# Optimization experiments

Measured on AMD Instinct MI355X. Metric: run time of the kernel, lower is better.

Reference implementation:

```python
import jax, jax.numpy as jnp
import numpy as np

D_MODEL = 512
NHEAD = 8


def setup_inputs() -> dict:
    key = jax.random.key(0)
    ks = jax.random.split(key, 8)
    d = D_MODEL
    low_feats = jax.random.normal(ks[0], (1, d, 32, 32), dtype=jnp.float32)
    guide_feats = jax.random.normal(ks[1], (1, d, 128, 128), dtype=jnp.float32)
    s = 1.0 / np.sqrt(d)
    Wq = jax.random.normal(ks[2], (d, d), dtype=jnp.float32) * s
    Wk = jax.random.normal(ks[3], (d, d), dtype=jnp.float32) * s
    Wv = jax.random.normal(ks[4], (d, d), dtype=jnp.float32) * s
    Wm = jax.random.normal(ks[5], (d, d), dtype=jnp.float32) * s
    gamma = jnp.ones((d,), dtype=jnp.float32)
    beta = jnp.zeros((d,), dtype=jnp.float32)
    return {"low_feats": low_feats, "guide_feats": guide_feats, "Wq": Wq,
            "Wk": Wk, "Wv": Wv, "Wm": Wm, "gamma": gamma, "beta": beta}


def _gather_windows(feat_hw, H, W):
    # feat_hw: [b, h, w, nhead, dim]. For each guide pixel (Y,X), nearest low
    # pixel is (Y*h//H, X*w//W) (PyTorch 'nearest'); gather its 3x3 neighborhood
    # with replicate padding (index clamping). Window order = ky*3+kx, matching
    # F.unfold channel layout. Returns [b, H*W, 9, nhead, dim].
    b, h, w, nh, dm = feat_hw.shape
    offs = jnp.array([-1, 0, 1])
    y0 = jnp.arange(H) * h // H                      # [H]
    x0 = jnp.arange(W) * w // W                      # [W]
    ys = jnp.clip(y0[:, None] + offs, 0, h - 1)      # [H,3] (ky)
    xs = jnp.clip(x0[:, None] + offs, 0, w - 1)      # [W,3] (kx)
    # -> [b, H, W, 3(ky), 3(kx), nhead, dim]
    g = feat_hw[:, ys[:, None, :, None], xs[None, :, None, :]]
    return g.reshape(b, H * W, 9, nh, dm)


def reference(low_feats, guide_feats, Wq, Wk, Wv, Wm, gamma, beta):
    b, d, H, W = guide_feats.shape
    _, _, h, w = low_feats.shape
    nh = NHEAD
    dm = d // nh
    g = guide_feats.transpose(0, 2, 3, 1).reshape(b, H * W, d)
    l = low_feats.transpose(0, 2, 3, 1).reshape(b, h * w, d)
    q = (g @ Wq.T).reshape(b, H * W, nh, dm)                 # [b,N,h,d]
    K = (l @ Wk.T).reshape(b, h, w, nh, dm)
    V = (l @ Wv.T).reshape(b, h, w, nh, dm)
    key = _gather_windows(K, H, W)                           # [b,N,9,h,d]
    val = _gather_windows(V, H, W)
    scale = 1.0 / jnp.sqrt(jnp.asarray(dm, dtype=q.dtype))
    # (q/sqrt(dm)) @ (k/sqrt(dm)) * sqrt(dm) == q@k / sqrt(dm)
    score = jnp.einsum('bnhd,bnkhd->bnhk', q, key) * scale
    attn = jax.nn.softmax(score, axis=-1)
    msg = jnp.einsum('bnhk,bnkhd->bnhd', attn, val).reshape(b, H * W, d)
    msg = msg @ Wm.T
    # LayerNorm(d_model), eps=1e-5
    mu = jnp.mean(msg, axis=-1, keepdims=True)
    var = jnp.mean((msg - mu) ** 2, axis=-1, keepdims=True)
    msg = (msg - mu) * jax.lax.rsqrt(var + 1e-5) * gamma + beta
    return msg.transpose(0, 2, 1).reshape(b, d, H, W)
```

## Files before the change

kernel.cpp:

```cpp
#include <hip/hip_runtime.h>
#include <hip/hip_bf16.h>
#include <stdint.h>

#define NQ 16384
#define NL 1024

typedef __bf16 bf16_t;
typedef __bf16 bf16x8 __attribute__((ext_vector_type(8)));
typedef __bf16 bf16x4 __attribute__((ext_vector_type(4)));
typedef float f32x4 __attribute__((ext_vector_type(4)));

__device__ __forceinline__ void gload_lds16(const void* g, void* l) {
  __builtin_amdgcn_global_load_lds(
      (const __attribute__((address_space(1))) uint32_t*)g,
      (__attribute__((address_space(3))) uint32_t*)l, 16, 0, 0);
}

__global__ __launch_bounds__(256) void cvt_all(const float* __restrict__ guide,
                                               const float* __restrict__ low,
                                               const float* __restrict__ Wq,
                                               const float* __restrict__ Wk,
                                               const float* __restrict__ Wv,
                                               const float* __restrict__ Wm,
                                               bf16_t* __restrict__ Gbf,
                                               bf16_t* __restrict__ Lbf,
                                               bf16_t* __restrict__ Wall) {
  const int bx = blockIdx.x, by = blockIdx.y, t = threadIdx.x;
  if (bx >= 544) {
    const int idx = (((bx - 544) * 16 + by) * 256 + t) * 4;
    const float* s;
    int off;
    if (idx < 262144)      { s = Wq; off = idx; }
    else if (idx < 524288) { s = Wk; off = idx - 262144; }
    else if (idx < 786432) { s = Wv; off = idx - 524288; }
    else                   { s = Wm; off = idx - 786432; }
    float4 v = *(const float4*)(s + off);
    bf16x4 o = {(bf16_t)v.x, (bf16_t)v.y, (bf16_t)v.z, (bf16_t)v.w};
    *(bf16x4*)(Wall + idx) = o;
    return;
  }
  __shared__ float tl[32][33];
  const float* src;
  bf16_t* dst;
  int ncols, n0;
  if (bx < 512) { src = guide; dst = Gbf; ncols = NQ; n0 = bx * 32; }
  else          { src = low;   dst = Lbf; ncols = NL; n0 = (bx - 512) * 32; }
  const int c0 = by * 32;
  const int c = t & 31, r = t >> 5;
#pragma unroll
  for (int it = 0; it < 4; ++it) {
    int rr = r + it * 8;
    tl[rr][c] = src[(size_t)(c0 + rr) * ncols + n0 + c];
  }
  __syncthreads();
#pragma unroll
  for (int it = 0; it < 4; ++it) {
    int rr = r + it * 8;
    dst[(size_t)(n0 + rr) * 512 + c0 + c] = (bf16_t)tl[c][rr];
  }
}

__global__ __launch_bounds__(256) void gemm_qkv(const bf16_t* __restrict__ G,
                                                const bf16_t* __restrict__ Wqb,
                                                bf16_t* __restrict__ Qo,
                                                const bf16_t* __restrict__ L,
                                                const bf16_t* __restrict__ Wkv,
                                                bf16_t* __restrict__ KVo) {
  __shared__ __align__(16) bf16_t As[2][128 * 64];
  __shared__ __align__(16) bf16_t Bs[2][128 * 64];
  const bf16_t *A, *B;
  bf16_t* C;
  int N, bm, bn;
  const int bid = blockIdx.x;
  if (bid < 512) { A = G; B = Wqb; C = Qo; N = 512; bm = (bid >> 2) * 128; bn = (bid & 3) * 128; }
  else { int id = bid - 512; A = L; B = Wkv; C = KVo; N = 1024; bm = (id >> 3) * 128; bn = (id & 7) * 128; }
  const int t = threadIdx.x;
  const int lane = t & 63;
  const int wave = t >> 6;
  const int wr = (wave >> 1) * 64;
  const int wc = (wave & 1) * 64;
  const int r0 = t >> 3;
  const int c0 = (t & 7) * 8;
  const int fr = lane & 15;
  const int fk = (lane >> 4) * 8;
#pragma unroll
  for (int it = 0; it < 4; ++it) {
    const int r = r0 + it * 32;
    gload_lds16(A + (size_t)(bm + r) * 512 + c0, &As[0][r * 64 + c0]);
    gload_lds16(B + (size_t)(bn + r) * 512 + c0, &Bs[0][r * 64 + c0]);
  }
  f32x4 acc[4][4] = {};
  __syncthreads();
#pragma unroll 2
  for (int kt = 0; kt < 8; ++kt) {
    const int cur = kt & 1;
    if (kt < 7) {
      const int k0 = (kt + 1) * 64;
#pragma unroll
      for (int it = 0; it < 4; ++it) {
        const int r = r0 + it * 32;
        gload_lds16(A + (size_t)(bm + r) * 512 + k0 + c0, &As[cur ^ 1][r * 64 + c0]);
        gload_lds16(B + (size_t)(bn + r) * 512 + k0 + c0, &Bs[cur ^ 1][r * 64 + c0]);
      }
    }
    __builtin_amdgcn_sched_barrier(0);
#pragma unroll
    for (int kk = 0; kk < 2; ++kk) {
      bf16x8 af[4], bfv[4];
#pragma unroll
      for (int i = 0; i < 4; ++i)
        af[i] = *(const bf16x8*)&As[cur][(wr + i * 16 + fr) * 64 + kk * 32 + fk];
#pragma unroll
      for (int i = 0; i < 4; ++i)
        bfv[i] = *(const bf16x8*)&Bs[cur][(wc + i * 16 + fr) * 64 + kk * 32 + fk];
#pragma unroll
      for (int i = 0; i < 4; ++i)
#pragma unroll
        for (int j = 0; j < 4; ++j)
          acc[i][j] = __builtin_amdgcn_mfma_f32_16x16x32_bf16(af[i], bfv[j], acc[i][j], 0, 0, 0);
    }
    __syncthreads();
  }
  const int crow = bm + wr + ((lane >> 4) * 4);
  const int ccol = bn + wc + fr;
#pragma unroll
  for (int i = 0; i < 4; ++i)
#pragma unroll
    for (int j = 0; j < 4; ++j) {
      const int row = crow + i * 16;
      const int col = ccol + j * 16;
#pragma unroll
      for (int v = 0; v < 4; ++v)
        C[(size_t)(row + v) * N + col] = (bf16_t)acc[i][j][v];
    }
}

__global__ __launch_bounds__(512) void attn_win(const bf16_t* __restrict__ Q,
                                                const bf16_t* __restrict__ KV,
                                                bf16_t* __restrict__ Msg) {
  __shared__ __align__(16) bf16_t Kl[9 * 512];
  __shared__ __align__(16) bf16_t Vl[9 * 512];
  const int t = threadIdx.x;
  const int lane = t & 63;
  const int wave = t >> 6;
  const int tile = blockIdx.x;
  const int ty = tile >> 5, tx = tile & 31;
  for (int kk = wave; kk < 9; kk += 8) {
    int ky = kk / 3, kx = kk - ky * 3;
    int yy = min(max(ty - 1 + ky, 0), 31);
    int xx = min(max(tx - 1 + kx, 0), 31);
    size_t p = (size_t)(yy * 32 + xx) * 1024;
    *(bf16x8*)&Kl[kk * 512 + lane * 8] = *(const bf16x8*)&KV[p + lane * 8];
    *(bf16x8*)&Vl[kk * 512 + lane * 8] = *(const bf16x8*)&KV[p + 512 + lane * 8];
  }
  __syncthreads();
  const int c = t & 3;
  const int h = (t >> 2) & 7;
  const int pl = t >> 5;
  const int y = ty * 4 + (pl >> 2), x = tx * 4 + (pl & 3);
  const size_t n = (size_t)y * 128 + x;
  const int doff = h * 64 + c * 16;
  const bf16x8 q0 = *(const bf16x8*)(Q + n * 512 + doff);
  const bf16x8 q1 = *(const bf16x8*)(Q + n * 512 + doff + 8);
  float s[9];
#pragma unroll
  for (int k = 0; k < 9; ++k) {
    bf16x8 k0 = *(const bf16x8*)&Kl[k * 512 + doff];
    bf16x8 k1 = *(const bf16x8*)&Kl[k * 512 + doff + 8];
    float p = 0.f;
#pragma unroll
    for (int e = 0; e < 8; ++e) p += (float)q0[e] * (float)k0[e] + (float)q1[e] * (float)k1[e];
    p += __shfl_xor(p, 1, 64);
    p += __shfl_xor(p, 2, 64);
    s[k] = p;
  }
  float mx = s[0];
#pragma unroll
  for (int k = 1; k < 9; ++k) mx = fmaxf(mx, s[k]);
  float sum = 0.f;
#pragma unroll
  for (int k = 0; k < 9; ++k) {
    s[k] = __expf((s[k] - mx) * 0.125f);
    sum += s[k];
  }
  const float inv = 1.0f / sum;
  float acc[16] = {};
#pragma unroll
  for (int k = 0; k < 9; ++k) {
    const float p = s[k] * inv;
    bf16x8 v0 = *(const bf16x8*)&Vl[k * 512 + doff];
    bf16x8 v1 = *(const bf16x8*)&Vl[k * 512 + doff + 8];
#pragma unroll
    for (int e = 0; e < 8; ++e) {
      acc[e] += p * (float)v0[e];
      acc[8 + e] += p * (float)v1[e];
    }
  }
  bf16x8 o0, o1;
#pragma unroll
  for (int e = 0; e < 8; ++e) { o0[e] = (bf16_t)acc[e]; o1[e] = (bf16_t)acc[8 + e]; }
  *(bf16x8*)(Msg + n * 512 + doff) = o0;
  *(bf16x8*)(Msg + n * 512 + doff + 8) = o1;
}

__global__ __launch_bounds__(512) void gemm_ln_out(const bf16_t* __restrict__ A,
                                                   const bf16_t* __restrict__ B,
                                                   const float* __restrict__ gamma,
                                                   const float* __restrict__ beta,
                                                   float* __restrict__ out) {
  __shared__ __align__(16) char smem[147456];
  __shared__ float2 part[64][4];
  __shared__ float2 st[64];
  bf16_t* const As0 = (bf16_t*)smem;
  bf16_t* const As1 = (bf16_t*)(smem + 8192);
  bf16_t* const Bs0 = (bf16_t*)(smem + 16384);
  bf16_t* const Bs1 = (bf16_t*)(smem + 81920);
  float* const Cl = (float*)smem;
  const int t = threadIdx.x;
  const int lane = t & 63;
  const int wave = t >> 6;
  const int wr = (wave >> 2) * 32;
  const int wc = (wave & 3) * 128;
  const int bm = blockIdx.x * 64;
  const int sr = t >> 3;
  const int sc = (t & 7) * 8;
  const int fr = lane & 15;
  const int fk = (lane >> 4) * 8;
  gload_lds16(A + (size_t)(bm + sr) * 512 + sc, &As0[sr * 64 + sc]);
#pragma unroll
  for (int it = 0; it < 8; ++it) {
    const int r = sr + it * 64;
    gload_lds16(B + (size_t)r * 512 + sc, &Bs0[r * 64 + sc]);
  }
  f32x4 acc[2][8] = {};
  __syncthreads();
#pragma unroll 2
  for (int kt = 0; kt < 8; ++kt) {
    bf16_t* const Asc = (kt & 1) ? As1 : As0;
    bf16_t* const Bsc = (kt & 1) ? Bs1 : Bs0;
    bf16_t* const Asn = (kt & 1) ? As0 : As1;
    bf16_t* const Bsn = (kt & 1) ? Bs0 : Bs1;
    if (kt < 7) {
      const int k0 = (kt + 1) * 64;
      gload_lds16(A + (size_t)(bm + sr) * 512 + k0 + sc, &Asn[sr * 64 + sc]);
#pragma unroll
      for (int it = 0; it < 8; ++it) {
        const int r = sr + it * 64;
        gload_lds16(B + (size_t)r * 512 + k0 + sc, &Bsn[r * 64 + sc]);
      }
    }
    __builtin_amdgcn_sched_barrier(0);
#pragma unroll
    for (int kk = 0; kk < 2; ++kk) {
      bf16x8 af[2], bfv[8];
#pragma unroll
      for (int i = 0; i < 2; ++i)
        af[i] = *(const bf16x8*)&Asc[(wr + i * 16 + fr) * 64 + kk * 32 + fk];
#pragma unroll
      for (int j = 0; j < 8; ++j)
        bfv[j] = *(const bf16x8*)&Bsc[(wc + j * 16 + fr) * 64 + kk * 32 + fk];
#pragma unroll
      for (int i = 0; i < 2; ++i)
#pragma unroll
        for (int j = 0; j < 8; ++j)
          acc[i][j] = __builtin_amdgcn_mfma_f32_16x16x32_bf16(af[i], bfv[j], acc[i][j], 0, 0, 0);
    }
    __syncthreads();
  }
#pragma unroll
  for (int i = 0; i < 2; ++i)
#pragma unroll
    for (int j = 0; j < 8; ++j) {
      const int row = wr + i * 16 + (lane >> 4) * 4;
      const int col = wc + j * 16 + fr;
#pragma unroll
      for (int v = 0; v < 4; ++v) Cl[(row + v) * 513 + col] = acc[i][j][v];
    }
#pragma unroll
  for (int i = 0; i < 2; ++i)
#pragma unroll
    for (int v = 0; v < 4; ++v) {
      float s = 0.f, s2 = 0.f;
#pragma unroll
      for (int j = 0; j < 8; ++j) {
        float x = acc[i][j][v];
        s += x;
        s2 += x * x;
      }
#pragma unroll
      for (int m = 1; m < 16; m <<= 1) {
        s += __shfl_xor(s, m, 64);
        s2 += __shfl_xor(s2, m, 64);
      }
      if ((lane & 15) == 0) {
        const int row = wr + i * 16 + (lane >> 4) * 4 + v;
        part[row][wave & 3] = make_float2(s, s2);
      }
    }
  __syncthreads();
  if (t < 64) {
    float2 p0 = part[t][0], p1 = part[t][1], p2 = part[t][2], p3 = part[t][3];
    float s = p0.x + p1.x + p2.x + p3.x;
    float s2 = p0.y + p1.y + p2.y + p3.y;
    float mu = s * (1.f / 512.f);
    float var = s2 * (1.f / 512.f) - mu * mu;
    st[t] = make_float2(mu, rsqrtf(var + 1e-5f));
  }
  __syncthreads();
  const int n = t & 63;
  const int j0 = t >> 6;
  const float2 ms = st[n];
#pragma unroll 8
  for (int jj = 0; jj < 64; ++jj) {
    const int j = j0 * 64 + jj;
    const float g = gamma[j], b = beta[j];
    const float x = Cl[n * 513 + j];
    out[(size_t)j * NQ + bm + n] = (x - ms.x) * ms.y * g + b;
  }
}

extern "C" void kernel_launch(void* const* d_in, const int* in_sizes, int n_in,
                              void* d_out, int out_size, void* d_ws, size_t ws_size,
                              hipStream_t stream) {
  const float* low = (const float*)d_in[0];
  const float* guide = (const float*)d_in[1];
  const float* Wq = (const float*)d_in[2];
  const float* Wk = (const float*)d_in[3];
  const float* Wv = (const float*)d_in[4];
  const float* Wm = (const float*)d_in[5];
  const float* gamma = (const float*)d_in[6];
  const float* beta = (const float*)d_in[7];
  float* out = (float*)d_out;

  char* w = (char*)d_ws;
  bf16_t* Gbf = (bf16_t*)w;  w += (size_t)NQ * 512 * 2;
  bf16_t* Lbf = (bf16_t*)w;  w += (size_t)NL * 512 * 2;
  bf16_t* Wall = (bf16_t*)w; w += (size_t)4 * 512 * 512 * 2;
  bf16_t* Qbf = (bf16_t*)w;  w += (size_t)NQ * 512 * 2;
  bf16_t* KVbf = (bf16_t*)w; w += (size_t)NL * 1024 * 2;
  bf16_t* Msg = (bf16_t*)w;  w += (size_t)NQ * 512 * 2;

  cvt_all<<<dim3(608, 16), 256, 0, stream>>>(guide, low, Wq, Wk, Wv, Wm, Gbf, Lbf, Wall);
  gemm_qkv<<<dim3(576), 256, 0, stream>>>(Gbf, Wall, Qbf, Lbf, Wall + 262144, KVbf);
  attn_win<<<dim3(1024), 512, 0, stream>>>(Qbf, KVbf, Msg);
  gemm_ln_out<<<dim3(NQ / 64), 512, 0, stream>>>(Msg, Wall + 786432, gamma, beta, out);
}
```

Before: 165.9 us.

## Merge QKV GEMM, window attention and output GEMM into one cooperative kernel

Replaces three separate launches with a single cooperative persistent kernel of 256 blocks that loops over jobs per stage, separated by grid-wide syncs. The QKV GEMM stage now uses 512-thread blocks with smaller per-wave tiles. The aim is to cut launch overhead and inter-kernel gaps. The trade-offs are grid.sync cost, the loss of overlap between stages, and one-block-per-CU occupancy, since the 147 KB shared buffer limits each stage's parallelism.

Result: slower. 355.6 us (+114.3%).

```diff
diff --git a/kernel.cpp b/kernel.cpp
--- a/kernel.cpp
+++ b/kernel.cpp
@@ -1,6 +1,9 @@
 #include <hip/hip_runtime.h>
+#include <hip/hip_cooperative_groups.h>
 #include <hip/hip_bf16.h>
 #include <stdint.h>
+
+namespace cg = cooperative_groups;
 
 #define NQ 16384
 #define NL 1024
@@ -60,262 +63,269 @@
   }
 }
 
-__global__ __launch_bounds__(256) void gemm_qkv(const bf16_t* __restrict__ G,
-                                                const bf16_t* __restrict__ Wqb,
-                                                bf16_t* __restrict__ Qo,
-                                                const bf16_t* __restrict__ L,
-                                                const bf16_t* __restrict__ Wkv,
-                                                bf16_t* __restrict__ KVo) {
-  __shared__ __align__(16) bf16_t As[2][128 * 64];
-  __shared__ __align__(16) bf16_t Bs[2][128 * 64];
-  const bf16_t *A, *B;
-  bf16_t* C;
-  int N, bm, bn;
+__global__ __launch_bounds__(512, 1) void mega(const bf16_t* __restrict__ Gbf,
+                                               const bf16_t* __restrict__ Lbf,
+                                               const bf16_t* __restrict__ Wall,
+                                               bf16_t* __restrict__ Qbf,
+                                               bf16_t* __restrict__ KVbf,
+                                               bf16_t* __restrict__ Msg,
+                                               const float* __restrict__ gamma,
+                                               const float* __restrict__ beta,
+                                               float* __restrict__ out) {
+  __shared__ __align__(16) char smem[147456];
+  __shared__ float2 part[64][4];
+  __shared__ float2 st[64];
+  cg::grid_group grid = cg::this_grid();
   const int bid = blockIdx.x;
-  if (bid < 512) { A = G; B = Wqb; C = Qo; N = 512; bm = (bid >> 2) * 128; bn = (bid & 3) * 128; }
-  else { int id = bid - 512; A = L; B = Wkv; C = KVo; N = 1024; bm = (id >> 3) * 128; bn = (id & 7) * 128; }
   const int t = threadIdx.x;
   const int lane = t & 63;
   const int wave = t >> 6;
-  const int wr = (wave >> 1) * 64;
-  const int wc = (wave & 1) * 64;
-  const int r0 = t >> 3;
-  const int c0 = (t & 7) * 8;
-  const int fr = lane & 15;
-  const int fk = (lane >> 4) * 8;
-#pragma unroll
-  for (int it = 0; it < 4; ++it) {
-    const int r = r0 + it * 32;
-    gload_lds16(A + (size_t)(bm + r) * 512 + c0, &As[0][r * 64 + c0]);
-    gload_lds16(B + (size_t)(bn + r) * 512 + c0, &Bs[0][r * 64 + c0]);
-  }
-  f32x4 acc[4][4] = {};
-  __syncthreads();
+
+  {
+    bf16_t* const As0 = (bf16_t*)smem;
+    bf16_t* const As1 = (bf16_t*)(smem + 16384);
+    bf16_t* const Bs0 = (bf16_t*)(smem + 32768);
+    bf16_t* const Bs1 = (bf16_t*)(smem + 49152);
+    const int r0 = t >> 3;
+    const int c0e = (t & 7) * 8;
+    const int wr = (wave >> 1) * 32;
+    const int wc = (wave & 1) * 64;
+    const int fr = lane & 15;
+    const int fk = (lane >> 4) * 8;
+    for (int job = bid; job < 576; job += 256) {
+      const bf16_t *A, *B;
+      bf16_t* C;
+      int N, bm, bn;
+      if (job < 512) { A = Gbf; B = Wall; C = Qbf; N = 512; bm = (job >> 2) * 128; bn = (job & 3) * 128; }
+      else { int j = job - 512; A = Lbf; B = Wall + 262144; C = KVbf; N = 1024; bm = (j >> 3) * 128; bn = (j & 7) * 128; }
+#pragma unroll
+      for (int it = 0; it < 2; ++it) {
+        const int r = r0 + it * 64;
+        gload_lds16(A + (size_t)(bm + r) * 512 + c0e, &As0[r * 64 + c0e]);
+        gload_lds16(B + (size_t)(bn + r) * 512 + c0e, &Bs0[r * 64 + c0e]);
+      }
+      f32x4 acc[2][4] = {};
+      __syncthreads();
 #pragma unroll 2
-  for (int kt = 0; kt < 8; ++kt) {
-    const int cur = kt & 1;
-    if (kt < 7) {
-      const int k0 = (kt + 1) * 64;
-#pragma unroll
-      for (int it = 0; it < 4; ++it) {
-        const int r = r0 + it * 32;
-        gload_lds16(A + (size_t)(bm + r) * 512 + k0 + c0, &As[cur ^ 1][r * 64 + c0]);
-        gload_lds16(B + (size_t)(bn + r) * 512 + k0 + c0, &Bs[cur ^ 1][r * 64 + c0]);
-      }
-    }
-    __builtin_amdgcn_sched_barrier(0);
-#pragma unroll
-    for (int kk = 0; kk < 2; ++kk) {
-      bf16x8 af[4], bfv[4];
-#pragma unroll
-      for (int i = 0; i < 4; ++i)
-        af[i] = *(const bf16x8*)&As[cur][(wr + i * 16 + fr) * 64 + kk * 32 + fk];
-#pragma unroll
-      for (int i = 0; i < 4; ++i)
-        bfv[i] = *(const bf16x8*)&Bs[cur][(wc + i * 16 + fr) * 64 + kk * 32 + fk];
-#pragma unroll
-      for (int i = 0; i < 4; ++i)
+      for (int kt = 0; kt < 8; ++kt) {
+        bf16_t* const Ac = (kt & 1) ? As1 : As0;
+        bf16_t* const Bc = (kt & 1) ? Bs1 : Bs0;
+        bf16_t* const An = (kt & 1) ? As0 : As1;
+        bf16_t* const Bn = (kt & 1) ? Bs0 : Bs1;
+        if (kt < 7) {
+          const int k0 = (kt + 1) * 64;
+#pragma unroll
+          for (int it = 0; it < 2; ++it) {
+            const int r = r0 + it * 64;
+            gload_lds16(A + (size_t)(bm + r) * 512 + k0 + c0e, &An[r * 64 + c0e]);
+            gload_lds16(B + (size_t)(bn + r) * 512 + k0 + c0e, &Bn[r * 64 + c0e]);
+          }
+        }
+        __builtin_amdgcn_sched_barrier(0);
+#pragma unroll
+        for (int kk = 0; kk < 2; ++kk) {
+          bf16x8 af[2], bv[4];
+#pragma unroll
+          for (int i = 0; i < 2; ++i)
+            af[i] = *(const bf16x8*)&Ac[(wr + i * 16 + fr) * 64 + kk * 32 + fk];
+#pragma unroll
+          for (int j = 0; j < 4; ++j)
+            bv[j] = *(const bf16x8*)&Bc[(wc + j * 16 + fr) * 64 + kk * 32 + fk];
+#pragma unroll
+          for (int i = 0; i < 2; ++i)
+#pragma unroll
+            for (int j = 0; j < 4; ++j)
+              acc[i][j] = __builtin_amdgcn_mfma_f32_16x16x32_bf16(af[i], bv[j], acc[i][j], 0, 0, 0);
+        }
+        __syncthreads();
+      }
+      const int crow = bm + wr + ((lane >> 4) * 4);
+      const int ccol = bn + wc + fr;
+#pragma unroll
+      for (int i = 0; i < 2; ++i)
 #pragma unroll
         for (int j = 0; j < 4; ++j)
-          acc[i][j] = __builtin_amdgcn_mfma_f32_16x16x32_bf16(af[i], bfv[j], acc[i][j], 0, 0, 0);
-    }
+#pragma unroll
+          for (int v = 0; v < 4; ++v)
+            C[(size_t)(crow + i * 16 + v) * N + ccol + j * 16] = (bf16_t)acc[i][j][v];
+    }
+  }
+  __threadfence();
+  grid.sync();
+
+  {
+    bf16_t* const Kl = (bf16_t*)smem;
+    bf16_t* const Vl = (bf16_t*)(smem + 9216);
+    for (int tile = bid; tile < 1024; tile += 256) {
+      const int ty = tile >> 5, tx = tile & 31;
+      for (int kk = wave; kk < 9; kk += 8) {
+        int ky = kk / 3, kx = kk - ky * 3;
+        int yy = min(max(ty - 1 + ky, 0), 31);
+        int xx = min(max(tx - 1 + kx, 0), 31);
+        size_t p = (size_t)(yy * 32 + xx) * 1024;
+        *(bf16x8*)&Kl[kk * 512 + lane * 8] = *(const bf16x8*)&KVbf[p + lane * 8];
+        *(bf16x8*)&Vl[kk * 512 + lane * 8] = *(const bf16x8*)&KVbf[p + 512 + lane * 8];
+      }
+      __syncthreads();
+      const int c = t & 3;
+      const int h = (t >> 2) & 7;
+      const int pl = t >> 5;
+      const int y = ty * 4 + (pl >> 2), x = tx * 4 + (pl & 3);
+      const size_t n = (size_t)y * 128 + x;
+      const int doff = h * 64 + c * 16;
+      const bf16x8 q0 = *(const bf16x8*)(Qbf + n * 512 + doff);
+      const bf16x8 q1 = *(const bf16x8*)(Qbf + n * 512 + doff + 8);
+      float s[9];
+#pragma unroll
+      for (int k = 0; k < 9; ++k) {
+        bf16x8 k0 = *(const bf16x8*)&Kl[k * 512 + doff];
+        bf16x8 k1 = *(const bf16x8*)&Kl[k * 512 + doff + 8];
+        float p = 0.f;
+#pragma unroll
+        for (int e = 0; e < 8; ++e) p += (float)q0[e] * (float)k0[e] + (float)q1[e] * (float)k1[e];
+        p += __shfl_xor(p, 1, 64);
+        p += __shfl_xor(p, 2, 64);
+        s[k] = p;
+      }
+      float mx = s[0];
+#pragma unroll
+      for (int k = 1; k < 9; ++k) mx = fmaxf(mx, s[k]);
+      float sum = 0.f;
+#pragma unroll
+      for (int k = 0; k < 9; ++k) {
+        s[k] = __expf((s[k] - mx) * 0.125f);
+        sum += s[k];
+      }
+      const float inv = 1.0f / sum;
+      float accv[16] = {};
+#pragma unroll
+      for (int k = 0; k < 9; ++k) {
+        const float p = s[k] * inv;
+        bf16x8 v0 = *(const bf16x8*)&Vl[k * 512 + doff];
+        bf16x8 v1 = *(const bf16x8*)&Vl[k * 512 + doff + 8];
+#pragma unroll
+        for (int e = 0; e < 8; ++e) {
+          accv[e] += p * (float)v0[e];
+          accv[8 + e] += p * (float)v1[e];
+        }
+      }
+      bf16x8 o0, o1;
+#pragma unroll
+      for (int e = 0; e < 8; ++e) { o0[e] = (bf16_t)accv[e]; o1[e] = (bf16_t)accv[8 + e]; }
+      *(bf16x8*)(Msg + n * 512 + doff) = o0;
+      *(bf16x8*)(Msg + n * 512 + doff + 8) = o1;
+      __syncthreads();
+    }
+  }
+  __threadfence();
+  grid.sync();
+
+  {
+    const bf16_t* const A = Msg;
+    const bf16_t* const B = Wall + 786432;
+    bf16_t* const As0 = (bf16_t*)smem;
+    bf16_t* const As1 = (bf16_t*)(smem + 8192);
+    bf16_t* const Bs0 = (bf16_t*)(smem + 16384);
+    bf16_t* const Bs1 = (bf16_t*)(smem + 81920);
+    float* const Cl = (float*)smem;
+    const int wr = (wave >> 2) * 32;
+    const int wc = (wave & 3) * 128;
+    const int bm = bid * 64;
+    const int sr = t >> 3;
+    const int sc = (t & 7) * 8;
+    const int fr = lane & 15;
+    const int fk = (lane >> 4) * 8;
+    gload_lds16(A + (size_t)(bm + sr) * 512 + sc, &As0[sr * 64 + sc]);
+#pragma unroll
+    for (int it = 0; it < 8; ++it) {
+      const int r = sr + it * 64;
+      gload_lds16(B + (size_t)r * 512 + sc, &Bs0[r * 64 + sc]);
+    }
+    f32x4 acc[2][8] = {};
     __syncthreads();
-  }
-  const int crow = bm + wr + ((lane >> 4) * 4);
-  const int ccol = bn + wc + fr;
-#pragma unroll
-  for (int i = 0; i < 4; ++i)
-#pragma unroll
-    for (int j = 0; j < 4; ++j) {
-      const int row = crow + i * 16;
-      const int col = ccol + j * 16;
-#pragma unroll
-      for (int v = 0; v < 4; ++v)
-        C[(size_t)(row + v) * N + col] = (bf16_t)acc[i][j][v];
-    }
-}
-
-__global__ __launch_bounds__(512) void attn_win(const bf16_t* __restrict__ Q,
-                                                const bf16_t* __restrict__ KV,
-                                                bf16_t* __restrict__ Msg) {
-  __shared__ __align__(16) bf16_t Kl[9 * 512];
-  __shared__ __align__(16) bf16_t Vl[9 * 512];
-  const int t = threadIdx.x;
-  const int lane = t & 63;
-  const int wave = t >> 6;
-  const int tile = blockIdx.x;
-  const int ty = tile >> 5, tx = tile & 31;
-  for (int kk = wave; kk < 9; kk += 8) {
-    int ky = kk / 3, kx = kk - ky * 3;
-    int yy = min(max(ty - 1 + ky, 0), 31);
-    int xx = min(max(tx - 1 + kx, 0), 31);
-    size_t p = (size_t)(yy * 32 + xx) * 1024;
-    *(bf16x8*)&Kl[kk * 512 + lane * 8] = *(const bf16x8*)&KV[p + lane * 8];
-    *(bf16x8*)&Vl[kk * 512 + lane * 8] = *(const bf16x8*)&KV[p + 512 + lane * 8];
-  }
-  __syncthreads();
-  const int c = t & 3;
-  const int h = (t >> 2) & 7;
-  const int pl = t >> 5;
-  const int y = ty * 4 + (pl >> 2), x = tx * 4 + (pl & 3);
-  const size_t n = (size_t)y * 128 + x;
-  const int doff = h * 64 + c * 16;
-  const bf16x8 q0 = *(const bf16x8*)(Q + n * 512 + doff);
-  const bf16x8 q1 = *(const bf16x8*)(Q + n * 512 + doff + 8);
-  float s[9];
-#pragma unroll
-  for (int k = 0; k < 9; ++k) {
-    bf16x8 k0 = *(const bf16x8*)&Kl[k * 512 + doff];
-    bf16x8 k1 = *(const bf16x8*)&Kl[k * 512 + doff + 8];
-    float p = 0.f;
-#pragma unroll
-    for (int e = 0; e < 8; ++e) p += (float)q0[e] * (float)k0[e] + (float)q1[e] * (float)k1[e];
-    p += __shfl_xor(p, 1, 64);
-    p += __shfl_xor(p, 2, 64);
-    s[k] = p;
-  }
-  float mx = s[0];
-#pragma unroll
-  for (int k = 1; k < 9; ++k) mx = fmaxf(mx, s[k]);
-  float sum = 0.f;
-#pragma unroll
-  for (int k = 0; k < 9; ++k) {
-    s[k] = __expf((s[k] - mx) * 0.125f);
-    sum += s[k];
-  }
-  const float inv = 1.0f / sum;
-  float acc[16] = {};
-#pragma unroll
-  for (int k = 0; k < 9; ++k) {
-    const float p = s[k] * inv;
-    bf16x8 v0 = *(const bf16x8*)&Vl[k * 512 + doff];
-    bf16x8 v1 = *(const bf16x8*)&Vl[k * 512 + doff + 8];
-#pragma unroll
-    for (int e = 0; e < 8; ++e) {
-      acc[e] += p * (float)v0[e];
-      acc[8 + e] += p * (float)v1[e];
-    }
-  }
-  bf16x8 o0, o1;
-#pragma unroll
-  for (int e = 0; e < 8; ++e) { o0[e] = (bf16_t)acc[e]; o1[e] = (bf16_t)acc[8 + e]; }
-  *(bf16x8*)(Msg + n * 512 + doff) = o0;
-  *(bf16x8*)(Msg + n * 512 + doff + 8) = o1;
-}
-
-__global__ __launch_bounds__(512) void gemm_ln_out(const bf16_t* __restrict__ A,
-                                                   const bf16_t* __restrict__ B,
-                                                   const float* __restrict__ gamma,
-                                                   const float* __restrict__ beta,
-                                                   float* __restrict__ out) {
-  __shared__ __align__(16) char smem[147456];
-  __shared__ float2 part[64][4];
-  __shared__ float2 st[64];
-  bf16_t* const As0 = (bf16_t*)smem;
-  bf16_t* const As1 = (bf16_t*)(smem + 8192);
-  bf16_t* const Bs0 = (bf16_t*)(smem + 16384);
-  bf16_t* const Bs1 = (bf16_t*)(smem + 81920);
-  float* const Cl = (float*)smem;
-  const int t = threadIdx.x;
-  const int lane = t & 63;
-  const int wave = t >> 6;
-  const int wr = (wave >> 2) * 32;
-  const int wc = (wave & 3) * 128;
-  const int bm = blockIdx.x * 64;
-  const int sr = t >> 3;
-  const int sc = (t & 7) * 8;
-  const int fr = lane & 15;
-  const int fk = (lane >> 4) * 8;
-  gload_lds16(A + (size_t)(bm + sr) * 512 + sc, &As0[sr * 64 + sc]);
-#pragma unroll
-  for (int it = 0; it < 8; ++it) {
-    const int r = sr + it * 64;
-    gload_lds16(B + (size_t)r * 512 + sc, &Bs0[r * 64 + sc]);
-  }
-  f32x4 acc[2][8] = {};
-  __syncthreads();
 #pragma unroll 2
-  for (int kt = 0; kt < 8; ++kt) {
-    bf16_t* const Asc = (kt & 1) ? As1 : As0;
-    bf16_t* const Bsc = (kt & 1) ? Bs1 : Bs0;
-    bf16_t* const Asn = (kt & 1) ? As0 : As1;
-    bf16_t* const Bsn = (kt & 1) ? Bs0 : Bs1;
-    if (kt < 7) {
-      const int k0 = (kt + 1) * 64;
-      gload_lds16(A + (size_t)(bm + sr) * 512 + k0 + sc, &Asn[sr * 64 + sc]);
-#pragma unroll
-      for (int it = 0; it < 8; ++it) {
-        const int r = sr + it * 64;
-        gload_lds16(B + (size_t)r * 512 + k0 + sc, &Bsn[r * 64 + sc]);
-      }
-    }
-    __builtin_amdgcn_sched_barrier(0);
-#pragma unroll
-    for (int kk = 0; kk < 2; ++kk) {
-      bf16x8 af[2], bfv[8];
-#pragma unroll
-      for (int i = 0; i < 2; ++i)
-        af[i] = *(const bf16x8*)&Asc[(wr + i * 16 + fr) * 64 + kk * 32 + fk];
-#pragma unroll
-      for (int j = 0; j < 8; ++j)
-        bfv[j] = *(const bf16x8*)&Bsc[(wc + j * 16 + fr) * 64 + kk * 32 + fk];
-#pragma unroll
-      for (int i = 0; i < 2; ++i)
+    for (int kt = 0; kt < 8; ++kt) {
+      bf16_t* const Asc = (kt & 1) ? As1 : As0;
+      bf16_t* const Bsc = (kt & 1) ? Bs1 : Bs0;
+      bf16_t* const Asn = (kt & 1) ? As0 : As1;
+      bf16_t* const Bsn = (kt & 1) ? Bs0 : Bs1;
+      if (kt < 7) {
+        const int k0 = (kt + 1) * 64;
+        gload_lds16(A + (size_t)(bm + sr) * 512 + k0 + sc, &Asn[sr * 64 + sc]);
+#pragma unroll
+        for (int it = 0; it < 8; ++it) {
+          const int r = sr + it * 64;
+          gload_lds16(B + (size_t)r * 512 + k0 + sc, &Bsn[r * 64 + sc]);
+        }
+      }
+      __builtin_amdgcn_sched_barrier(0);
+#pragma unroll
+      for (int kk = 0; kk < 2; ++kk) {
+        bf16x8 af[2], bfv[8];
+#pragma unroll
+        for (int i = 0; i < 2; ++i)
+          af[i] = *(const bf16x8*)&Asc[(wr + i * 16 + fr) * 64 + kk * 32 + fk];
 #pragma unroll
         for (int j = 0; j < 8; ++j)
-          acc[i][j] = __builtin_amdgcn_mfma_f32_16x16x32_bf16(af[i], bfv[j], acc[i][j], 0, 0, 0);
-    }
+          bfv[j] = *(const bf16x8*)&Bsc[(wc + j * 16 + fr) * 64 + kk * 32 + fk];
+#pragma unroll
+        for (int i = 0; i < 2; ++i)
+#pragma unroll
+          for (int j = 0; j < 8; ++j)
+            acc[i][j] = __builtin_amdgcn_mfma_f32_16x16x32_bf16(af[i], bfv[j], acc[i][j], 0, 0, 0);
+      }
+      __syncthreads();
+    }
+#pragma unroll
+    for (int i = 0; i < 2; ++i)
+#pragma unroll
+      for (int j = 0; j < 8; ++j) {
+        const int row = wr + i * 16 + (lane >> 4) * 4;
+        const int col = wc + j * 16 + fr;
+#pragma unroll
+        for (int v = 0; v < 4; ++v) Cl[(row + v) * 513 + col] = acc[i][j][v];
+      }
+#pragma unroll
+    for (int i = 0; i < 2; ++i)
+#pragma unroll
+      for (int v = 0; v < 4; ++v) {
+        float s = 0.f, s2 = 0.f;
+#pragma unroll
+        for (int j = 0; j < 8; ++j) {
+          float x = acc[i][j][v];
+          s += x;
+          s2 += x * x;
+        }
+#pragma unroll
+        for (int m = 1; m < 16; m <<= 1) {
+          s += __shfl_xor(s, m, 64);
+          s2 += __shfl_xor(s2, m, 64);
+        }
+        if ((lane & 15) == 0) {
+          const int row = wr + i * 16 + (lane >> 4) * 4 + v;
+          part[row][wave & 3] = make_float2(s, s2);
+        }
+      }
     __syncthreads();
-  }
-#pragma unroll
-  for (int i = 0; i < 2; ++i)
-#pragma unroll
-    for (int j = 0; j < 8; ++j) {
-      const int row = wr + i * 16 + (lane >> 4) * 4;
-      const int col = wc + j * 16 + fr;
-#pragma unroll
-      for (int v = 0; v < 4; ++v) Cl[(row + v) * 513 + col] = acc[i][j][v];
-    }
-#pragma unroll
-  for (int i = 0; i < 2; ++i)
-#pragma unroll
-    for (int v = 0; v < 4; ++v) {
-      float s = 0.f, s2 = 0.f;
-#pragma unroll
-      for (int j = 0; j < 8; ++j) {
-        float x = acc[i][j][v];
-        s += x;
-        s2 += x * x;
-      }
-#pragma unroll
-      for (int m = 1; m < 16; m <<= 1) {
-        s += __shfl_xor(s, m, 64);
-        s2 += __shfl_xor(s2, m, 64);
-      }
-      if ((lane & 15) == 0) {
-        const int row = wr + i * 16 + (lane >> 4) * 4 + v;
-        part[row][wave & 3] = make_float2(s, s2);
-      }
-    }
-  __syncthreads();
-  if (t < 64) {
-    float2 p0 = part[t][0], p1 = part[t][1], p2 = part[t][2], p3 = part[t][3];
-    float s = p0.x + p1.x + p2.x + p3.x;
-    float s2 = p0.y + p1.y + p2.y + p3.y;
-    float mu = s * (1.f / 512.f);
-    float var = s2 * (1.f / 512.f) - mu * mu;
-    st[t] = make_float2(mu, rsqrtf(var + 1e-5f));
-  }
-  __syncthreads();
-  const int n = t & 63;
-  const int j0 = t >> 6;
-  const float2 ms = st[n];
+    if (t < 64) {
+      float2 p0 = part[t][0], p1 = part[t][1], p2 = part[t][2], p3 = part[t][3];
+      float s = p0.x + p1.x + p2.x + p3.x;
+      float s2 = p0.y + p1.y + p2.y + p3.y;
+      float mu = s * (1.f / 512.f);
+      float var = s2 * (1.f / 512.f) - mu * mu;
+      st[t] = make_float2(mu, rsqrtf(var + 1e-5f));
+    }
+    __syncthreads();
+    const int n = t & 63;
+    const int j0 = t >> 6;
+    const float2 ms = st[n];
 #pragma unroll 8
-  for (int jj = 0; jj < 64; ++jj) {
-    const int j = j0 * 64 + jj;
-    const float g = gamma[j], b = beta[j];
-    const float x = Cl[n * 513 + j];
-    out[(size_t)j * NQ + bm + n] = (x - ms.x) * ms.y * g + b;
+    for (int jj = 0; jj < 64; ++jj) {
+      const int j = j0 * 64 + jj;
+      const float g = gamma[j], b = beta[j];
+      const float x = Cl[n * 513 + j];
+      out[(size_t)j * NQ + bm + n] = (x - ms.x) * ms.y * g + b;
+    }
   }
 }
 
@@ -341,7 +351,12 @@
   bf16_t* Msg = (bf16_t*)w;  w += (size_t)NQ * 512 * 2;
 
   cvt_all<<<dim3(608, 16), 256, 0, stream>>>(guide, low, Wq, Wk, Wv, Wm, Gbf, Lbf, Wall);
-  gemm_qkv<<<dim3(576), 256, 0, stream>>>(Gbf, Wall, Qbf, Lbf, Wall + 262144, KVbf);
-  attn_win<<<dim3(1024), 512, 0, stream>>>(Qbf, KVbf, Msg);
-  gemm_ln_out<<<dim3(NQ / 64), 512, 0, stream>>>(Msg, Wall + 786432, gamma, beta, out);
+
+  const bf16_t* Gbf_c = Gbf;
+  const bf16_t* Lbf_c = Lbf;
+  const bf16_t* Wall_c = Wall;
+  void* args[] = {(void*)&Gbf_c, (void*)&Lbf_c, (void*)&Wall_c,
+                  (void*)&Qbf, (void*)&KVbf, (void*)&Msg,
+                  (void*)&gamma, (void*)&beta, (void*)&out};
+  hipLaunchCooperativeKernel((void*)mega, dim3(256), dim3(512), args, 0, stream);
 }
```

## Swizzle QKV GEMM LDS layout and retile output GEMM with register-direct LayerNorm store

Applied to the files above, without the earlier changes.

The QKV GEMM now XOR-swizzles the 16-byte chunk position within each 64-wide LDS row, permuting global source columns on load and applying the matching slot on read, to cut LDS bank conflicts in the MFMA fragment loads. The output GEMM+LayerNorm kernel is retiled from 64 rows with K-step 64 to 32 rows with K-step 32. Its LDS footprint shrinks from about 147 KB to about 68 KB, which may let more blocks reside per CU. The fp32 LDS staging of C is dropped, and normalized values are written straight from accumulators as float4 stores along the transposed output. The risk is that each block now reloads the full 512x512 Wm for only 32 rows, doubling weight traffic through L2, and the K loop runs twice as many synchronised iterations.

New measurement: 162.8 us. No clear change (-1.9%).

```diff
diff --git a/kernel.cpp b/kernel.cpp
--- a/kernel.cpp
+++ b/kernel.cpp
@@ -60,7 +60,7 @@
   }
 }
 
-__global__ __launch_bounds__(256) void gemm_qkv(const bf16_t* __restrict__ G,
+__global__ __launch_bounds__(256) void gemm_qkv(const bf16_t* __restrict__ G_,
                                                 const bf16_t* __restrict__ Wqb,
                                                 bf16_t* __restrict__ Qo,
                                                 const bf16_t* __restrict__ L,
@@ -72,7 +72,7 @@
   bf16_t* C;
   int N, bm, bn;
   const int bid = blockIdx.x;
-  if (bid < 512) { A = G; B = Wqb; C = Qo; N = 512; bm = (bid >> 2) * 128; bn = (bid & 3) * 128; }
+  if (bid < 512) { A = G_; B = Wqb; C = Qo; N = 512; bm = (bid >> 2) * 128; bn = (bid & 3) * 128; }
   else { int id = bid - 512; A = L; B = Wkv; C = KVo; N = 1024; bm = (id >> 3) * 128; bn = (id & 7) * 128; }
   const int t = threadIdx.x;
   const int lane = t & 63;
@@ -81,13 +81,15 @@
   const int wc = (wave & 1) * 64;
   const int r0 = t >> 3;
   const int c0 = (t & 7) * 8;
+  const int sgc = (((t & 7) ^ ((t >> 3) & 7)) << 3);
   const int fr = lane & 15;
-  const int fk = (lane >> 4) * 8;
+  const int G = lane >> 4;
+  const int f7 = fr & 7;
 #pragma unroll
   for (int it = 0; it < 4; ++it) {
     const int r = r0 + it * 32;
-    gload_lds16(A + (size_t)(bm + r) * 512 + c0, &As[0][r * 64 + c0]);
-    gload_lds16(B + (size_t)(bn + r) * 512 + c0, &Bs[0][r * 64 + c0]);
+    gload_lds16(A + (size_t)(bm + r) * 512 + sgc, &As[0][r * 64 + c0]);
+    gload_lds16(B + (size_t)(bn + r) * 512 + sgc, &Bs[0][r * 64 + c0]);
   }
   f32x4 acc[4][4] = {};
   __syncthreads();
@@ -99,20 +101,21 @@
 #pragma unroll
       for (int it = 0; it < 4; ++it) {
         const int r = r0 + it * 32;
-        gload_lds16(A + (size_t)(bm + r) * 512 + k0 + c0, &As[cur ^ 1][r * 64 + c0]);
-        gload_lds16(B + (size_t)(bn + r) * 512 + k0 + c0, &Bs[cur ^ 1][r * 64 + c0]);
+        gload_lds16(A + (size_t)(bm + r) * 512 + k0 + sgc, &As[cur ^ 1][r * 64 + c0]);
+        gload_lds16(B + (size_t)(bn + r) * 512 + k0 + sgc, &Bs[cur ^ 1][r * 64 + c0]);
       }
     }
     __builtin_amdgcn_sched_barrier(0);
 #pragma unroll
     for (int kk = 0; kk < 2; ++kk) {
+      const int slot = (((kk * 4 + G) ^ f7) << 3);
       bf16x8 af[4], bfv[4];
 #pragma unroll
       for (int i = 0; i < 4; ++i)
-        af[i] = *(const bf16x8*)&As[cur][(wr + i * 16 + fr) * 64 + kk * 32 + fk];
+        af[i] = *(const bf16x8*)&As[cur][(wr + i * 16 + fr) * 64 + slot];
 #pragma unroll
       for (int i = 0; i < 4; ++i)
-        bfv[i] = *(const bf16x8*)&Bs[cur][(wc + i * 16 + fr) * 64 + kk * 32 + fk];
+        bfv[i] = *(const bf16x8*)&Bs[cur][(wc + i * 16 + fr) * 64 + slot];
 #pragma unroll
       for (int i = 0; i < 4; ++i)
 #pragma unroll
@@ -121,7 +124,7 @@
     }
     __syncthreads();
   }
-  const int crow = bm + wr + ((lane >> 4) * 4);
+  const int crow = bm + wr + (G * 4);
   const int ccol = bn + wc + fr;
 #pragma unroll
   for (int i = 0; i < 4; ++i)
@@ -208,81 +211,61 @@
                                                    const float* __restrict__ gamma,
                                                    const float* __restrict__ beta,
                                                    float* __restrict__ out) {
-  __shared__ __align__(16) char smem[147456];
-  __shared__ float2 part[64][4];
-  __shared__ float2 st[64];
-  bf16_t* const As0 = (bf16_t*)smem;
-  bf16_t* const As1 = (bf16_t*)(smem + 8192);
-  bf16_t* const Bs0 = (bf16_t*)(smem + 16384);
-  bf16_t* const Bs1 = (bf16_t*)(smem + 81920);
-  float* const Cl = (float*)smem;
+  __shared__ __align__(16) bf16_t As[2][32 * 32];
+  __shared__ __align__(16) bf16_t Bs[2][512 * 32];
+  __shared__ float2 part[32][8];
+  __shared__ float2 st[32];
   const int t = threadIdx.x;
   const int lane = t & 63;
   const int wave = t >> 6;
-  const int wr = (wave >> 2) * 32;
-  const int wc = (wave & 3) * 128;
-  const int bm = blockIdx.x * 64;
-  const int sr = t >> 3;
-  const int sc = (t & 7) * 8;
+  const int wc = wave * 64;
+  const int bm = blockIdx.x * 32;
   const int fr = lane & 15;
-  const int fk = (lane >> 4) * 8;
-  gload_lds16(A + (size_t)(bm + sr) * 512 + sc, &As0[sr * 64 + sc]);
-#pragma unroll
-  for (int it = 0; it < 8; ++it) {
-    const int r = sr + it * 64;
-    gload_lds16(B + (size_t)r * 512 + sc, &Bs0[r * 64 + sc]);
-  }
-  f32x4 acc[2][8] = {};
-  __syncthreads();
-#pragma unroll 2
-  for (int kt = 0; kt < 8; ++kt) {
-    bf16_t* const Asc = (kt & 1) ? As1 : As0;
-    bf16_t* const Bsc = (kt & 1) ? Bs1 : Bs0;
-    bf16_t* const Asn = (kt & 1) ? As0 : As1;
-    bf16_t* const Bsn = (kt & 1) ? Bs0 : Bs1;
-    if (kt < 7) {
-      const int k0 = (kt + 1) * 64;
-      gload_lds16(A + (size_t)(bm + sr) * 512 + k0 + sc, &Asn[sr * 64 + sc]);
-#pragma unroll
-      for (int it = 0; it < 8; ++it) {
-        const int r = sr + it * 64;
-        gload_lds16(B + (size_t)r * 512 + k0 + sc, &Bsn[r * 64 + sc]);
+  const int G = lane >> 4;
+  const int sr = t >> 2;
+  const int sc = (t & 3) * 8;
+  if (t < 128) gload_lds16(A + (size_t)(bm + sr) * 512 + sc, &As[0][sr * 32 + sc]);
+#pragma unroll
+  for (int it = 0; it < 4; ++it) {
+    const int r = sr + it * 128;
+    gload_lds16(B + (size_t)r * 512 + sc, &Bs[0][r * 32 + sc]);
+  }
+  f32x4 acc[2][4] = {};
+  __syncthreads();
+#pragma unroll 4
+  for (int kt = 0; kt < 16; ++kt) {
+    const int cur = kt & 1;
+    if (kt < 15) {
+      const int k0 = (kt + 1) * 32;
+      if (t < 128) gload_lds16(A + (size_t)(bm + sr) * 512 + k0 + sc, &As[cur ^ 1][sr * 32 + sc]);
+#pragma unroll
+      for (int it = 0; it < 4; ++it) {
+        const int r = sr + it * 128;
+        gload_lds16(B + (size_t)r * 512 + k0 + sc, &Bs[cur ^ 1][r * 32 + sc]);
       }
     }
     __builtin_amdgcn_sched_barrier(0);
-#pragma unroll
-    for (int kk = 0; kk < 2; ++kk) {
-      bf16x8 af[2], bfv[8];
-#pragma unroll
-      for (int i = 0; i < 2; ++i)
-        af[i] = *(const bf16x8*)&Asc[(wr + i * 16 + fr) * 64 + kk * 32 + fk];
-#pragma unroll
-      for (int j = 0; j < 8; ++j)
-        bfv[j] = *(const bf16x8*)&Bsc[(wc + j * 16 + fr) * 64 + kk * 32 + fk];
-#pragma unroll
-      for (int i = 0; i < 2; ++i)
-#pragma unroll
-        for (int j = 0; j < 8; ++j)
-          acc[i][j] = __builtin_amdgcn_mfma_f32_16x16x32_bf16(af[i], bfv[j], acc[i][j], 0, 0, 0);
-    }
+    bf16x8 af[2], bv[4];
+#pragma unroll
+    for (int i = 0; i < 2; ++i)
+      af[i] = *(const bf16x8*)&As[cur][(i * 16 + fr) * 32 + G * 8];
+#pragma unroll
+    for (int j = 0; j < 4; ++j)
+      bv[j] = *(const bf16x8*)&Bs[cur][(wc + j * 16 + fr) * 32 + G * 8];
+#pragma unroll
+    for (int i = 0; i < 2; ++i)
+#pragma unroll
+      for (int j = 0; j < 4; ++j)
+        acc[i][j] = __builtin_amdgcn_mfma_f32_16x16x32_bf16(af[i], bv[j], acc[i][j], 0, 0, 0);
     __syncthreads();
   }
-#pragma unroll
-  for (int i = 0; i < 2; ++i)
-#pragma unroll
-    for (int j = 0; j < 8; ++j) {
-      const int row = wr + i * 16 + (lane >> 4) * 4;
-      const int col = wc + j * 16 + fr;
-#pragma unroll
-      for (int v = 0; v < 4; ++v) Cl[(row + v) * 513 + col] = acc[i][j][v];
-    }
 #pragma unroll
   for (int i = 0; i < 2; ++i)
 #pragma unroll
     for (int v = 0; v < 4; ++v) {
       float s = 0.f, s2 = 0.f;
 #pragma unroll
-      for (int j = 0; j < 8; ++j) {
+      for (int j = 0; j < 4; ++j) {
         float x = acc[i][j][v];
         s += x;
         s2 += x * x;
@@ -292,30 +275,40 @@
         s += __shfl_xor(s, m, 64);
         s2 += __shfl_xor(s2, m, 64);
       }
-      if ((lane & 15) == 0) {
-        const int row = wr + i * 16 + (lane >> 4) * 4 + v;
-        part[row][wave & 3] = make_float2(s, s2);
-      }
-    }
-  __syncthreads();
-  if (t < 64) {
-    float2 p0 = part[t][0], p1 = part[t][1], p2 = part[t][2], p3 = part[t][3];
-    float s = p0.x + p1.x + p2.x + p3.x;
-    float s2 = p0.y + p1.y + p2.y + p3.y;
+      if (fr == 0) part[i * 16 + G * 4 + v][wave] = make_float2(s, s2);
+    }
+  __syncthreads();
+  if (t < 32) {
+    float s = 0.f, s2 = 0.f;
+#pragma unroll
+    for (int w = 0; w < 8; ++w) {
+      float2 p = part[t][w];
+      s += p.x;
+      s2 += p.y;
+    }
     float mu = s * (1.f / 512.f);
     float var = s2 * (1.f / 512.f) - mu * mu;
     st[t] = make_float2(mu, rsqrtf(var + 1e-5f));
   }
   __syncthreads();
-  const int n = t & 63;
-  const int j0 = t >> 6;
-  const float2 ms = st[n];
-#pragma unroll 8
-  for (int jj = 0; jj < 64; ++jj) {
-    const int j = j0 * 64 + jj;
-    const float g = gamma[j], b = beta[j];
-    const float x = Cl[n * 513 + j];
-    out[(size_t)j * NQ + bm + n] = (x - ms.x) * ms.y * g + b;
+  float2 ms[2][4];
+#pragma unroll
+  for (int i = 0; i < 2; ++i)
+#pragma unroll
+    for (int v = 0; v < 4; ++v) ms[i][v] = st[i * 16 + G * 4 + v];
+#pragma unroll
+  for (int j = 0; j < 4; ++j) {
+    const int jg = wc + j * 16 + fr;
+    const float g = gamma[jg], b = beta[jg];
+#pragma unroll
+    for (int i = 0; i < 2; ++i) {
+      float4 o;
+      o.x = (acc[i][j][0] - ms[i][0].x) * ms[i][0].y * g + b;
+      o.y = (acc[i][j][1] - ms[i][1].x) * ms[i][1].y * g + b;
+      o.z = (acc[i][j][2] - ms[i][2].x) * ms[i][2].y * g + b;
+      o.w = (acc[i][j][3] - ms[i][3].x) * ms[i][3].y * g + b;
+      *(float4*)(out + (size_t)jg * NQ + bm + i * 16 + G * 4) = o;
+    }
   }
 }
 
@@ -343,5 +336,5 @@
   cvt_all<<<dim3(608, 16), 256, 0, stream>>>(guide, low, Wq, Wk, Wv, Wm, Gbf, Lbf, Wall);
   gemm_qkv<<<dim3(576), 256, 0, stream>>>(Gbf, Wall, Qbf, Lbf, Wall + 262144, KVbf);
   attn_win<<<dim3(1024), 512, 0, stream>>>(Qbf, KVbf, Msg);
-  gemm_ln_out<<<dim3(NQ / 64), 512, 0, stream>>>(Msg, Wall + 786432, gamma, beta, out);
-}
+  gemm_ln_out<<<dim3(NQ / 32), 512, 0, stream>>>(Msg, Wall + 786432, gamma, beta, out);
+}
```
